# Performance work log

Hardware: AMD Instinct MI355X
Metric: run time of the kernel (lower is better)

Reference implementation:

```python
import jax, jax.numpy as jnp
import numpy as np

MARGIN = 0.2


def setup_inputs() -> dict:
    key = jax.random.key(0)
    k1, k2 = jax.random.split(key)
    B, D, C = 4096, 512, 512
    embeddings = jax.random.normal(k1, (B, D), dtype=jnp.float32)
    labels = jax.random.randint(k2, (B,), 0, C, dtype=jnp.int64)
    return {"embeddings": embeddings, "labels": labels}


def reference(embeddings, labels):
    B = embeddings.shape[0]
    # L2-normalize rows (eps matches torch F.normalize default 1e-12)
    norm = jnp.maximum(jnp.linalg.norm(embeddings, axis=1, keepdims=True), 1e-12)
    e = embeddings / norm
    # cosine distance matrix [B, B]
    dist = 1.0 - e @ e.T
    same = labels[:, None] == labels[None, :]
    eye = jnp.eye(B, dtype=bool)
    pos_mask = same & ~eye
    neg_mask = ~same
    # dist in [0, 2]; sentinels outside that range for masked reductions
    hardest_pos = jnp.max(jnp.where(pos_mask, dist, -1.0), axis=1)
    hardest_neg = jnp.min(jnp.where(neg_mask, dist, 3.0), axis=1)
    valid = jnp.any(pos_mask, axis=1) & jnp.any(neg_mask, axis=1)
    per_anchor = jax.nn.relu(hardest_pos - hardest_neg + MARGIN)
    loss_sum = jnp.sum(jnp.where(valid, per_anchor, 0.0))
    n_valid = jnp.maximum(jnp.sum(valid.astype(jnp.int32)), 1)
    return loss_sum / n_valid.astype(embeddings.dtype)
```

## Files before the change

### kernel.cpp

```cpp
#include <hip/hip_runtime.h>
#include <hip/hip_bf16.h>

#define BDIM 4096
#define DDIM 512
#define BT 128
#define NKT 8
#define NPAN (BDIM / BT)
#define GRIDX (NPAN * NPAN)

typedef __bf16 bf16x8 __attribute__((ext_vector_type(8)));
typedef float f32x4 __attribute__((ext_vector_type(4)));
typedef unsigned short ushort_t;

__device__ inline ushort_t f2bf(float f) {
  __hip_bfloat16 h = __float2bfloat16(f);
  return *reinterpret_cast<ushort_t*>(&h);
}

__device__ inline unsigned int enc_f32(float x) {
  unsigned int u = __float_as_uint(x);
  return (u & 0x80000000u) ? ~u : (u | 0x80000000u);
}
__device__ inline float dec_f32(unsigned int e) {
  unsigned int u = (e & 0x80000000u) ? (e ^ 0x80000000u) : ~e;
  return __uint_as_float(u);
}

__global__ __launch_bounds__(256) void norm_kernel(const float* __restrict__ x,
                                                   ushort_t* __restrict__ e,
                                                   unsigned int* __restrict__ minpos_e,
                                                   unsigned int* __restrict__ maxneg_e) {
  if (blockIdx.x == 0) {
    const unsigned int init_min = enc_f32(1e30f);
    const unsigned int init_max = enc_f32(-1e30f);
    for (int i = threadIdx.x; i < BDIM; i += 256) {
      minpos_e[i] = init_min;
      maxneg_e[i] = init_max;
    }
  }
  const int row  = blockIdx.x * 4 + (threadIdx.x >> 6);
  const int lane = threadIdx.x & 63;
  const float4* xr = reinterpret_cast<const float4*>(x + (size_t)row * DDIM);
  float4 v0 = xr[lane];
  float4 v1 = xr[lane + 64];
  float ss = v0.x*v0.x + v0.y*v0.y + v0.z*v0.z + v0.w*v0.w
           + v1.x*v1.x + v1.y*v1.y + v1.z*v1.z + v1.w*v1.w;
#pragma unroll
  for (int off = 32; off >= 1; off >>= 1) ss += __shfl_xor(ss, off);
  const float inv = 1.0f / fmaxf(sqrtf(ss), 1e-12f);

  ushort4 p0, p1;
  p0.x = f2bf(v0.x * inv); p0.y = f2bf(v0.y * inv);
  p0.z = f2bf(v0.z * inv); p0.w = f2bf(v0.w * inv);
  p1.x = f2bf(v1.x * inv); p1.y = f2bf(v1.y * inv);
  p1.z = f2bf(v1.z * inv); p1.w = f2bf(v1.w * inv);
  ushort4* er = reinterpret_cast<ushort4*>(e + (size_t)row * DDIM);
  er[lane]      = p0;
  er[lane + 64] = p1;
}

#define STAGE(buf, kt)                                                         \
  do {                                                                         \
    _Pragma("unroll")                                                          \
    for (int q = 0; q < 8; ++q) {                                              \
      const int off  = q * 4096 + tid * 16;                      \
      const int loff = off & 16383;                                            \
      const int row  = loff >> 7;                                              \
      const int kb   = loff & 127;                                             \
      const int pan  = (q < 4) ? Ibase : Jbase;                                \
      const char* src = (const char*)e + (size_t)(pan + row) * (DDIM * 2) +    \
                        (kt) * 128 + (kb ^ ((row & 7) << 4));                  \
      __builtin_amdgcn_global_load_lds(                                        \
          (const __attribute__((address_space(1))) void*)src,                  \
          (__attribute__((address_space(3))) void*)(&Blds[buf][off]),          \
          16, 0, 0);                                                           \
    }                                                                          \
  } while (0)

__global__ __launch_bounds__(256, 2) void gemm_reduce_kernel(
    const ushort_t* __restrict__ e, const int* __restrict__ labels,
    unsigned int* __restrict__ minpos_e, unsigned int* __restrict__ maxneg_e) {
  __shared__ __align__(16) char Blds[2][32768];
  __shared__ int Llab[256];

  const int tid  = threadIdx.x;
  const int wave = tid >> 6;
  const int lane = tid & 63;
  const int l15  = lane & 15;
  const int g    = lane >> 4;
  const int wr   = wave >> 1;
  const int wc   = wave & 1;

  const int bid  = blockIdx.x;
  const int sbid = (bid & 7) * (GRIDX / 8) + (bid >> 3);
  const int Ibase = (sbid >> 5) * BT;
  const int Jbase = (sbid & 31) * BT;

  if (tid < 128) Llab[tid] = labels[Ibase + tid];
  else           Llab[tid] = labels[Jbase + tid - 128];

  f32x4 acc[4][4];
#pragma unroll
  for (int m = 0; m < 4; ++m)
#pragma unroll
    for (int n = 0; n < 4; ++n) acc[m][n] = (f32x4){0.f, 0.f, 0.f, 0.f};

  STAGE(0, 0);
  __syncthreads();

  for (int kt = 0; kt < NKT; ++kt) {
    if (kt + 1 < NKT) STAGE((kt + 1) & 1, kt + 1);

    const char* Ab = Blds[kt & 1];
    const char* Bb = Blds[kt & 1] + 16384;
#pragma unroll
    for (int kk = 0; kk < 2; ++kk) {
      bf16x8 a[4], b[4];
#pragma unroll
      for (int m = 0; m < 4; ++m) {
        const int row = wr * 64 + m * 16 + l15;
        a[m] = *reinterpret_cast<const bf16x8*>(
            Ab + row * 128 + ((kk * 64 + g * 16) ^ ((row & 7) << 4)));
      }
#pragma unroll
      for (int n = 0; n < 4; ++n) {
        const int row = wc * 64 + n * 16 + l15;
        b[n] = *reinterpret_cast<const bf16x8*>(
            Bb + row * 128 + ((kk * 64 + g * 16) ^ ((row & 7) << 4)));
      }
#pragma unroll
      for (int m = 0; m < 4; ++m)
#pragma unroll
        for (int n = 0; n < 4; ++n)
          acc[m][n] = __builtin_amdgcn_mfma_f32_16x16x32_bf16(a[m], b[n],
                                                              acc[m][n], 0, 0, 0);
    }
    __syncthreads();
  }

  float cmp[4], cmx[4];
  int lj[4], gj[4];
#pragma unroll
  for (int n = 0; n < 4; ++n) {
    cmp[n] = 1e30f; cmx[n] = -1e30f;
    gj[n]  = Jbase + wc * 64 + n * 16 + l15;
    lj[n]  = Llab[128 + wc * 64 + n * 16 + l15];
  }
#pragma unroll
  for (int m = 0; m < 4; ++m) {
#pragma unroll
    for (int r = 0; r < 4; ++r) {
      const int rloc = wr * 64 + m * 16 + g * 4 + r;
      const int li   = Llab[rloc];
      const int gi   = Ibase + rloc;
#pragma unroll
      for (int n = 0; n < 4; ++n) {
        const float v = acc[m][n][r];
        if (li == lj[n]) {
          if (gi != gj[n]) cmp[n] = fminf(cmp[n], v);
        } else {
          cmx[n] = fmaxf(cmx[n], v);
        }
      }
    }
  }
#pragma unroll
  for (int off = 16; off <= 32; off <<= 1) {
#pragma unroll
    for (int n = 0; n < 4; ++n) {
      cmp[n] = fminf(cmp[n], __shfl_xor(cmp[n], off));
      cmx[n] = fmaxf(cmx[n], __shfl_xor(cmx[n], off));
    }
  }
  if (g == 0) {
#pragma unroll
    for (int n = 0; n < 4; ++n) {
      if (cmp[n] < 1e29f)  atomicMin(&minpos_e[gj[n]], enc_f32(cmp[n]));
      if (cmx[n] > -1e29f) atomicMax(&maxneg_e[gj[n]], enc_f32(cmx[n]));
    }
  }
}

__global__ __launch_bounds__(1024) void finalize_kernel(
    const unsigned int* __restrict__ minpos_e, const unsigned int* __restrict__ maxneg_e,
    float* __restrict__ out) {
  const int tid = threadIdx.x;
  float sum = 0.f;
  int cnt = 0;
  for (int row = tid; row < BDIM; row += 1024) {
    const float mp = dec_f32(minpos_e[row]);
    const float mn = dec_f32(maxneg_e[row]);
    if (mp < 1e29f && mn > -1e29f) {
      sum += fmaxf(0.f, mn - mp + 0.2f);
      cnt += 1;
    }
  }
#pragma unroll
  for (int off = 32; off >= 1; off >>= 1) {
    sum += __shfl_xor(sum, off);
    cnt += __shfl_xor(cnt, off);
  }
  __shared__ float wsum[16];
  __shared__ int   wcnt[16];
  const int wv = tid >> 6, ln = tid & 63;
  if (ln == 0) { wsum[wv] = sum; wcnt[wv] = cnt; }
  __syncthreads();
  if (tid == 0) {
    float S = 0.f; int C = 0;
    for (int w = 0; w < 16; ++w) { S += wsum[w]; C += wcnt[w]; }
    out[0] = S / (float)(C > 0 ? C : 1);
  }
}

extern "C" void kernel_launch(void* const* d_in, const int* in_sizes, int n_in,
                              void* d_out, int out_size, void* d_ws, size_t ws_size,
                              hipStream_t stream) {
  const float* x      = (const float*)d_in[0];
  const int*   labels = (const int*)d_in[1];
  float* out = (float*)d_out;

  char* ws = (char*)d_ws;
  ushort_t* e            = (ushort_t*)ws;
  unsigned int* minpos_e = (unsigned int*)(ws + (size_t)BDIM * DDIM * 2);
  unsigned int* maxneg_e = minpos_e + BDIM;

  norm_kernel<<<BDIM / 4, 256, 0, stream>>>(x, e, minpos_e, maxneg_e);
  gemm_reduce_kernel<<<GRIDX, 256, 0, stream>>>(e, labels, minpos_e, maxneg_e);
  finalize_kernel<<<1, 1024, 0, stream>>>(minpos_e, maxneg_e, out);
}
```

Baseline: 36.82 us.

## Exploit Gram matrix symmetry: compute upper-triangular tiles, reduce rows and columns

The grid now covers only the upper-triangular 128x128 tile pairs of the symmetric similarity matrix instead of all tile pairs. Each tile reduces both column-wise and row-wise, so the masked min and max reach the anchors of both panels. Tile indices come from a float sqrt with integer correction loops, and blocks stay interleaved for L2 locality. This roughly halves the MFMA and LDS-load work, at the cost of extra row shuffles, more atomics, and diagonal tiles that do the same work as off-diagonal ones.

```diff
diff --git a/kernel.cpp b/kernel.cpp
--- a/kernel.cpp
+++ b/kernel.cpp
@@ -6,7 +6,7 @@
 #define BT 128
 #define NKT 8
 #define NPAN (BDIM / BT)
-#define GRIDX (NPAN * NPAN)
+#define NTRI (NPAN * (NPAN + 1) / 2)
 
 typedef __bf16 bf16x8 __attribute__((ext_vector_type(8)));
 typedef float f32x4 __attribute__((ext_vector_type(4)));
@@ -91,10 +91,14 @@
   const int wr   = wave >> 1;
   const int wc   = wave & 1;
 
-  const int bid  = blockIdx.x;
-  const int sbid = (bid & 7) * (GRIDX / 8) + (bid >> 3);
-  const int Ibase = (sbid >> 5) * BT;
-  const int Jbase = (sbid & 31) * BT;
+  const int bid = blockIdx.x;
+  const int t   = (bid & 7) * (NTRI / 8) + (bid >> 3);
+  int I = (int)((65.0f - sqrtf(4225.0f - 8.0f * (float)t)) * 0.5f);
+  while (32 * (I + 1) - ((I + 1) * I) / 2 <= t) ++I;
+  while (32 * I - (I * (I - 1)) / 2 > t) --I;
+  const int J = I + (t - (32 * I - (I * (I - 1)) / 2));
+  const int Ibase = I * BT;
+  const int Jbase = J * BT;
 
   if (tid < 128) Llab[tid] = labels[Ibase + tid];
   else           Llab[tid] = labels[Jbase + tid - 128];
@@ -146,6 +150,12 @@
     gj[n]  = Jbase + wc * 64 + n * 16 + l15;
     lj[n]  = Llab[128 + wc * 64 + n * 16 + l15];
   }
+  float rmp[4][4], rmx[4][4];
+#pragma unroll
+  for (int m = 0; m < 4; ++m)
+#pragma unroll
+    for (int r = 0; r < 4; ++r) { rmp[m][r] = 1e30f; rmx[m][r] = -1e30f; }
+
 #pragma unroll
   for (int m = 0; m < 4; ++m) {
 #pragma unroll
@@ -157,13 +167,18 @@
       for (int n = 0; n < 4; ++n) {
         const float v = acc[m][n][r];
         if (li == lj[n]) {
-          if (gi != gj[n]) cmp[n] = fminf(cmp[n], v);
+          if (gi != gj[n]) {
+            rmp[m][r] = fminf(rmp[m][r], v);
+            cmp[n]    = fminf(cmp[n], v);
+          }
         } else {
-          cmx[n] = fmaxf(cmx[n], v);
+          rmx[m][r] = fmaxf(rmx[m][r], v);
+          cmx[n]    = fmaxf(cmx[n], v);
         }
       }
     }
   }
+
 #pragma unroll
   for (int off = 16; off <= 32; off <<= 1) {
 #pragma unroll
@@ -172,12 +187,33 @@
       cmx[n] = fmaxf(cmx[n], __shfl_xor(cmx[n], off));
     }
   }
+#pragma unroll
+  for (int off = 1; off < 16; off <<= 1) {
+#pragma unroll
+    for (int m = 0; m < 4; ++m)
+#pragma unroll
+      for (int r = 0; r < 4; ++r) {
+        rmp[m][r] = fminf(rmp[m][r], __shfl_xor(rmp[m][r], off));
+        rmx[m][r] = fmaxf(rmx[m][r], __shfl_xor(rmx[m][r], off));
+      }
+  }
+
   if (g == 0) {
 #pragma unroll
     for (int n = 0; n < 4; ++n) {
       if (cmp[n] < 1e29f)  atomicMin(&minpos_e[gj[n]], enc_f32(cmp[n]));
       if (cmx[n] > -1e29f) atomicMax(&maxneg_e[gj[n]], enc_f32(cmx[n]));
     }
+  }
+  if (l15 == 0) {
+#pragma unroll
+    for (int m = 0; m < 4; ++m)
+#pragma unroll
+      for (int r = 0; r < 4; ++r) {
+        const int gi = Ibase + wr * 64 + m * 16 + g * 4 + r;
+        if (rmp[m][r] < 1e29f)  atomicMin(&minpos_e[gi], enc_f32(rmp[m][r]));
+        if (rmx[m][r] > -1e29f) atomicMax(&maxneg_e[gi], enc_f32(rmx[m][r]));
+      }
   }
 }
 
@@ -225,6 +261,6 @@
   unsigned int* maxneg_e = minpos_e + BDIM;
 
   norm_kernel<<<BDIM / 4, 256, 0, stream>>>(x, e, minpos_e, maxneg_e);
-  gemm_reduce_kernel<<<GRIDX, 256, 0, stream>>>(e, labels, minpos_e, maxneg_e);
+  gemm_reduce_kernel<<<NTRI, 256, 0, stream>>>(e, labels, minpos_e, maxneg_e);
   finalize_kernel<<<1, 1024, 0, stream>>>(minpos_e, maxneg_e, out);
 }
```

After: 45.49 us. +23.6%, slower.
